# Performance work log

Measured on AMD Instinct MI355X. Metric: run time of the kernel, lower is better.

Reference implementation:

```python
import jax, jax.numpy as jnp
import numpy as np

B, N_IN, D_IN = 64, 2304, 8
J, L = 32, 16  # num_capsules, capsule_dim
ROUTING_ITERS = 3
EPS = 1e-7


def setup_inputs() -> dict:
    key = jax.random.key(0)
    k1, k2 = jax.random.split(key)
    x = jax.random.normal(k1, (B, N_IN, D_IN), dtype=jnp.float32)
    W = jax.random.normal(k2, (N_IN, J, D_IN, L), dtype=jnp.float32) * 0.05
    return {"x": x, "W": W}


def squash(s):
    # s: [B, J, L]
    sq_norm = jnp.sum(jnp.square(s), axis=-1, keepdims=True)
    scale = sq_norm / (1.0 + sq_norm) / jnp.sqrt(sq_norm + EPS)
    return scale * s


def reference(x, W):
    # Faithful to the source: einsum 'bni,njkl->bnjl' sums i and k independently.
    predictions = jnp.einsum('bni,njkl->bnjl', x, W)  # [B, N, J, L]
    b = jnp.zeros((x.shape[0], N_IN, J), dtype=predictions.dtype)
    v = None
    for i in range(ROUTING_ITERS):
        c = jax.nn.softmax(b, axis=2)                       # [B, N, J]
        s = jnp.sum(predictions * c[..., None], axis=1)     # [B, J, L]
        v = squash(s)                                       # [B, J, L]
        if i < ROUTING_ITERS - 1:
            agreement = jnp.einsum('bnjl,bjl->bnj', predictions, v)
            b = b + agreement
    return v
```

## Files before the change

kernel.cpp:

```cpp
#include <hip/hip_runtime.h>

#define B_   64
#define N_   2304
#define J_   32
#define L_   16
#define EPS_ 1e-7f
#define BG   4
#define NSPL 32
#define NSL  72
#define NGRID (NSPL * (B_ / BG))
#define NTHR 1024
#define NT   9
#define STR  20


__global__ __launch_bounds__(256) void prep_kernel(const float* __restrict__ x,
                                                   const float* __restrict__ W,
                                                   float* __restrict__ Ws,
                                                   float* __restrict__ xs_g) {
    const int o = blockIdx.x * 256 + threadIdx.x;
    const int NW4 = N_ * J_ * L_ / 4;
    if (o < NW4) {
        const int n = o >> 7, r = o & 127;
        const float4* base = (const float4*)W + (size_t)n * 1024 + (r >> 2) * 32 + (r & 3);
        float4 s = make_float4(0.f, 0.f, 0.f, 0.f);
#pragma unroll
        for (int k = 0; k < 8; ++k) {
            float4 t = base[k * 4];
            s.x += t.x; s.y += t.y; s.z += t.z; s.w += t.w;
        }
        ((float4*)Ws)[o] = s;
    } else {
        const int q = o - NW4;
        if (q < B_ * N_) {
            const float4* p4 = (const float4*)(x + (size_t)q * 8);
            float4 a = p4[0], c = p4[1];
            xs_g[q] = a.x + a.y + a.z + a.w + c.x + c.y + c.z + c.w;
        }
    }
}

template<int T>
__global__ __launch_bounds__(NTHR) void iter_kernel(const float* __restrict__ Ws,
                                                    const float* __restrict__ xs_g,
                                                    const float* __restrict__ pA,
                                                    float* __restrict__ s0g,
                                                    float* __restrict__ pout) {
    __shared__ float xs_lds[BG * NSL];
    __shared__ float u_lds[BG * 544];
    __shared__ float sred[512 * STR];

    const int tid = threadIdx.x;
    const int sp  = blockIdx.x & (NSPL - 1);
    const int bg  = blockIdx.x >> 5;
    const int bb  = bg * BG;
    const int nb  = sp * NSL;

    if (tid < BG * NSL) {
        const int b4f = tid / NSL, nlf = tid - b4f * NSL;
        xs_lds[tid] = xs_g[(size_t)(bb + b4f) * N_ + nb + nlf];
    }

    if constexpr (T == 1) {
        for (int q = tid; q < BG * 512; q += NTHR) {
            const int ob = q >> 9, jl = q & 511;
            const float* pp = pA + ((size_t)(bb + ob) * NSPL) * 512 + jl;
            float s = 0.f;
#pragma unroll
            for (int s2i = 0; s2i < NSPL; ++s2i) s += pp[s2i * 512];
            if (sp == 0) s0g[(bb + ob) * 512 + jl] = s;
            float sq = s * s;
#pragma unroll
            for (int off = 1; off <= 8; off <<= 1) sq += __shfl_xor(sq, off);
            u_lds[ob * 544 + (jl >> 4) * 17 + (jl & 15)] =
                s * (sq / (1.f + sq) / sqrtf(sq + EPS_));
        }
    } else if constexpr (T == 2) {
        for (int q = tid; q < BG * 512; q += NTHR) {
            const int ob = q >> 9, jl = q & 511;
            float s = s0g[(bb + ob) * 512 + jl];
            float sq = s * s;
#pragma unroll
            for (int off = 1; off <= 8; off <<= 1) sq += __shfl_xor(sq, off);
            float u = s * (sq / (1.f + sq) / sqrtf(sq + EPS_));
            const float* pp = pA + ((size_t)(bb + ob) * NSPL) * 512 + jl;
            float s1 = 0.f;
#pragma unroll
            for (int s2i = 0; s2i < NSPL; ++s2i) s1 += pp[s2i * 512];
            float sq1 = s1 * s1;
#pragma unroll
            for (int off = 1; off <= 8; off <<= 1) sq1 += __shfl_xor(sq1, off);
            u += s1 * (sq1 / (1.f + sq1) / sqrtf(sq1 + EPS_));
            u_lds[ob * 544 + (jl >> 4) * 17 + (jl & 15)] = u;
        }
    }
    __syncthreads();

    const int nl8 = tid >> 7;
    const int b4  = (tid >> 5) & 3;
    const int j   = tid & 31;

    float u4[16];
    if constexpr (T > 0) {
#pragma unroll
        for (int l = 0; l < 16; ++l) u4[l] = u_lds[b4 * 544 + j * 17 + l];
    }

    float acc[16];
#pragma unroll
    for (int l = 0; l < 16; ++l) acc[l] = 0.f;

    const float* wbase = Ws + (size_t)nb * 512 + j * 16;
    const float* xbase = xs_lds + b4 * NSL;

    for (int tile = 0; tile < NT; ++tile) {
        const int nl = tile * 8 + nl8;
        const float4* wr = (const float4*)(wbase + (size_t)nl * 512);
        float4 w0 = wr[0], w1 = wr[1], w2 = wr[2], w3 = wr[3];
        const float xsv = xbase[nl];
        float wgt;
        if constexpr (T == 0) {
            wgt = xsv * (1.f / 32.f);
        } else {
            float lg = w0.x*u4[0]  + w0.y*u4[1]  + w0.z*u4[2]  + w0.w*u4[3]
                     + w1.x*u4[4]  + w1.y*u4[5]  + w1.z*u4[6]  + w1.w*u4[7]
                     + w2.x*u4[8]  + w2.y*u4[9]  + w2.z*u4[10] + w2.w*u4[11]
                     + w3.x*u4[12] + w3.y*u4[13] + w3.z*u4[14] + w3.w*u4[15];
            lg *= xsv;
            float e = __expf(lg);
            float ss = e;
#pragma unroll
            for (int off = 1; off <= 16; off <<= 1) ss += __shfl_xor(ss, off);
            wgt = (e / ss) * xsv;
        }
        acc[0]  += wgt*w0.x; acc[1]  += wgt*w0.y; acc[2]  += wgt*w0.z; acc[3]  += wgt*w0.w;
        acc[4]  += wgt*w1.x; acc[5]  += wgt*w1.y; acc[6]  += wgt*w1.z; acc[7]  += wgt*w1.w;
        acc[8]  += wgt*w2.x; acc[9]  += wgt*w2.y; acc[10] += wgt*w2.z; acc[11] += wgt*w2.w;
        acc[12] += wgt*w3.x; acc[13] += wgt*w3.y; acc[14] += wgt*w3.z; acc[15] += wgt*w3.w;
    }

    if (nl8 >= 4) {
        float* sr = sred + (size_t)(tid - 512) * STR;
        ((float4*)sr)[0] = make_float4(acc[0],  acc[1],  acc[2],  acc[3]);
        ((float4*)sr)[1] = make_float4(acc[4],  acc[5],  acc[6],  acc[7]);
        ((float4*)sr)[2] = make_float4(acc[8],  acc[9],  acc[10], acc[11]);
        ((float4*)sr)[3] = make_float4(acc[12], acc[13], acc[14], acc[15]);
    }
    __syncthreads();
    if (nl8 < 4) {
        float* sr = sred + (size_t)tid * STR;
#pragma unroll
        for (int d = 0; d < 4; ++d) {
            float4 t = ((float4*)sr)[d];
            t.x += acc[d*4+0]; t.y += acc[d*4+1]; t.z += acc[d*4+2]; t.w += acc[d*4+3];
            ((float4*)sr)[d] = t;
        }
    }
    __syncthreads();

    for (int q = tid; q < BG * 512; q += NTHR) {
        const int ob = q >> 9, jl = q & 511;
        const int oj = jl >> 4, ol = jl & 15;
        float s = 0.f;
#pragma unroll
        for (int nl = 0; nl < 4; ++nl)
            s += sred[(size_t)(nl * 128 + ob * 32 + oj) * STR + ol];
        pout[((size_t)(bb + ob) * NSPL + sp) * 512 + jl] = s;
    }
}

__global__ __launch_bounds__(512) void final_kernel(const float* __restrict__ p2,
                                                    float* __restrict__ out) {
    const int g = blockIdx.x * 512 + threadIdx.x;
    const int b = g >> 9, jl = g & 511;
    const float* pp = p2 + ((size_t)b * NSPL) * 512 + jl;
    float s = 0.f;
#pragma unroll
    for (int s2 = 0; s2 < NSPL; ++s2) s += pp[s2 * 512];
    float sq = s * s;
#pragma unroll
    for (int off = 1; off <= 8; off <<= 1) sq += __shfl_xor(sq, off);
    out[g] = s * (sq / (1.f + sq) / sqrtf(sq + EPS_));
}

extern "C" void kernel_launch(void* const* d_in, const int* in_sizes, int n_in,
                              void* d_out, int out_size, void* d_ws, size_t ws_size,
                              hipStream_t stream) {
    const float* x = (const float*)d_in[0];
    const float* W = (const float*)d_in[1];
    float* out = (float*)d_out;

    float* Ws  = (float*)d_ws;
    float* xsg = Ws  + (size_t)N_ * J_ * L_;
    float* p0  = xsg + (size_t)B_ * N_;
    float* p1  = p0  + (size_t)B_ * NSPL * 512;
    float* p2  = p1  + (size_t)B_ * NSPL * 512;
    float* s0  = p2  + (size_t)B_ * NSPL * 512;

    prep_kernel<<<1728, 256, 0, stream>>>(x, W, Ws, xsg);
    iter_kernel<0><<<NGRID, NTHR, 0, stream>>>(Ws, xsg, nullptr, nullptr, p0);
    iter_kernel<1><<<NGRID, NTHR, 0, stream>>>(Ws, xsg, p0, s0, p1);
    iter_kernel<2><<<NGRID, NTHR, 0, stream>>>(Ws, xsg, p1, s0, p2);
    final_kernel<<<64, 512, 0, stream>>>(p2, out);
}
```

Baseline: 91.30 us.

## Halve N-splits, prefetch W rows, fuse final reduction via last-block atomic counter

New measurement: 100.6 us. 1.1x slower.

```diff
diff --git a/kernel.cpp b/kernel.cpp
--- a/kernel.cpp
+++ b/kernel.cpp
@@ -6,19 +6,23 @@
 #define L_   16
 #define EPS_ 1e-7f
 #define BG   4
-#define NSPL 32
-#define NSL  72
-#define NGRID (NSPL * (B_ / BG))
+#define NSPL 16
+#define NSL  144
 #define NTHR 1024
-#define NT   9
+#define NT   18
 #define STR  20
 
 
 __global__ __launch_bounds__(256) void prep_kernel(const float* __restrict__ x,
                                                    const float* __restrict__ W,
                                                    float* __restrict__ Ws,
-                                                   float* __restrict__ xs_g) {
+                                                   float* __restrict__ xs_g,
+                                                   float* __restrict__ p2z,
+                                                   int* __restrict__ ctr) {
     const int o = blockIdx.x * 256 + threadIdx.x;
+    if (o == 0) *ctr = 0;
+    if (o < (B_ * NSPL * 512) / 4)
+        ((float4*)p2z)[o] = make_float4(0.f, 0.f, 0.f, 0.f);
     const int NW4 = N_ * J_ * L_ / 4;
     if (o < NW4) {
         const int n = o >> 7, r = o & 127;
@@ -45,14 +49,18 @@
                                                     const float* __restrict__ xs_g,
                                                     const float* __restrict__ pA,
                                                     float* __restrict__ s0g,
-                                                    float* __restrict__ pout) {
+                                                    float* __restrict__ pout,
+                                                    int* __restrict__ ctr,
+                                                    float* __restrict__ out) {
     __shared__ float xs_lds[BG * NSL];
     __shared__ float u_lds[BG * 544];
     __shared__ float sred[512 * STR];
+    __shared__ int lastflag;
 
     const int tid = threadIdx.x;
-    const int sp  = blockIdx.x & (NSPL - 1);
-    const int bg  = blockIdx.x >> 5;
+    const int blk = blockIdx.x;
+    const int sp  = ((blk & 7) << 1) | ((blk >> 3) & 1);
+    const int bg  = blk >> 4;
     const int bb  = bg * BG;
     const int nb  = sp * NSL;
 
@@ -60,6 +68,14 @@
         const int b4f = tid / NSL, nlf = tid - b4f * NSL;
         xs_lds[tid] = xs_g[(size_t)(bb + b4f) * N_ + nb + nlf];
     }
+
+    const int nl8 = tid >> 7;
+    const int b4  = (tid >> 5) & 3;
+    const int j   = tid & 31;
+    const float* wbase = Ws + (size_t)nb * 512 + j * 16;
+
+    const float4* wr0 = (const float4*)(wbase + (size_t)nl8 * 512);
+    float4 w0 = wr0[0], w1 = wr0[1], w2 = wr0[2], w3 = wr0[3];
 
     if constexpr (T == 1) {
         for (int q = tid; q < BG * 512; q += NTHR) {
@@ -67,7 +83,7 @@
             const float* pp = pA + ((size_t)(bb + ob) * NSPL) * 512 + jl;
             float s = 0.f;
 #pragma unroll
-            for (int s2i = 0; s2i < NSPL; ++s2i) s += pp[s2i * 512];
+            for (int i = 0; i < NSPL; ++i) s += pp[i * 512];
             if (sp == 0) s0g[(bb + ob) * 512 + jl] = s;
             float sq = s * s;
 #pragma unroll
@@ -86,7 +102,7 @@
             const float* pp = pA + ((size_t)(bb + ob) * NSPL) * 512 + jl;
             float s1 = 0.f;
 #pragma unroll
-            for (int s2i = 0; s2i < NSPL; ++s2i) s1 += pp[s2i * 512];
+            for (int i = 0; i < NSPL; ++i) s1 += pp[i * 512];
             float sq1 = s1 * s1;
 #pragma unroll
             for (int off = 1; off <= 8; off <<= 1) sq1 += __shfl_xor(sq1, off);
@@ -96,10 +112,6 @@
     }
     __syncthreads();
 
-    const int nl8 = tid >> 7;
-    const int b4  = (tid >> 5) & 3;
-    const int j   = tid & 31;
-
     float u4[16];
     if constexpr (T > 0) {
 #pragma unroll
@@ -110,14 +122,15 @@
 #pragma unroll
     for (int l = 0; l < 16; ++l) acc[l] = 0.f;
 
-    const float* wbase = Ws + (size_t)nb * 512 + j * 16;
     const float* xbase = xs_lds + b4 * NSL;
 
     for (int tile = 0; tile < NT; ++tile) {
-        const int nl = tile * 8 + nl8;
-        const float4* wr = (const float4*)(wbase + (size_t)nl * 512);
-        float4 w0 = wr[0], w1 = wr[1], w2 = wr[2], w3 = wr[3];
-        const float xsv = xbase[nl];
+        float4 n0, n1, n2, n3;
+        if (tile + 1 < NT) {
+            const float4* nx = (const float4*)(wbase + (size_t)((tile + 1) * 8 + nl8) * 512);
+            n0 = nx[0]; n1 = nx[1]; n2 = nx[2]; n3 = nx[3];
+        }
+        const float xsv = xbase[tile * 8 + nl8];
         float wgt;
         if constexpr (T == 0) {
             wgt = xsv * (1.f / 32.f);
@@ -137,6 +150,7 @@
         acc[4]  += wgt*w1.x; acc[5]  += wgt*w1.y; acc[6]  += wgt*w1.z; acc[7]  += wgt*w1.w;
         acc[8]  += wgt*w2.x; acc[9]  += wgt*w2.y; acc[10] += wgt*w2.z; acc[11] += wgt*w2.w;
         acc[12] += wgt*w3.x; acc[13] += wgt*w3.y; acc[14] += wgt*w3.z; acc[15] += wgt*w3.w;
+        if (tile + 1 < NT) { w0 = n0; w1 = n1; w2 = n2; w3 = n3; }
     }
 
     if (nl8 >= 4) {
@@ -165,22 +179,35 @@
 #pragma unroll
         for (int nl = 0; nl < 4; ++nl)
             s += sred[(size_t)(nl * 128 + ob * 32 + oj) * STR + ol];
-        pout[((size_t)(bb + ob) * NSPL + sp) * 512 + jl] = s;
-    }
-}
-
-__global__ __launch_bounds__(512) void final_kernel(const float* __restrict__ p2,
-                                                    float* __restrict__ out) {
-    const int g = blockIdx.x * 512 + threadIdx.x;
-    const int b = g >> 9, jl = g & 511;
-    const float* pp = p2 + ((size_t)b * NSPL) * 512 + jl;
-    float s = 0.f;
-#pragma unroll
-    for (int s2 = 0; s2 < NSPL; ++s2) s += pp[s2 * 512];
-    float sq = s * s;
-#pragma unroll
-    for (int off = 1; off <= 8; off <<= 1) sq += __shfl_xor(sq, off);
-    out[g] = s * (sq / (1.f + sq) / sqrtf(sq + EPS_));
+        if constexpr (T < 2)
+            pout[((size_t)(bb + ob) * NSPL + sp) * 512 + jl] = s;
+        else
+            unsafeAtomicAdd(&pout[((size_t)(bb + ob) * NSPL + sp) * 512 + jl], s);
+    }
+
+    if constexpr (T == 2) {
+        __syncthreads();
+        if (tid == 0) {
+            int old = __hip_atomic_fetch_add(ctr, 1, __ATOMIC_RELAXED,
+                                             __HIP_MEMORY_SCOPE_AGENT);
+            lastflag = (old == 255) ? 1 : 0;
+        }
+        __syncthreads();
+        if (lastflag) {
+            for (int r = tid; r < B_ * 512; r += NTHR) {
+                const int b = r >> 9, jl = r & 511;
+                float s = 0.f;
+#pragma unroll
+                for (int spp = 0; spp < NSPL; ++spp)
+                    s += __hip_atomic_load(&pout[((size_t)b * NSPL + spp) * 512 + jl],
+                                           __ATOMIC_RELAXED, __HIP_MEMORY_SCOPE_AGENT);
+                float sq = s * s;
+#pragma unroll
+                for (int off = 1; off <= 8; off <<= 1) sq += __shfl_xor(sq, off);
+                out[r] = s * (sq / (1.f + sq) / sqrtf(sq + EPS_));
+            }
+        }
+    }
 }
 
 extern "C" void kernel_launch(void* const* d_in, const int* in_sizes, int n_in,
@@ -196,10 +223,10 @@
     float* p1  = p0  + (size_t)B_ * NSPL * 512;
     float* p2  = p1  + (size_t)B_ * NSPL * 512;
     float* s0  = p2  + (size_t)B_ * NSPL * 512;
-
-    prep_kernel<<<1728, 256, 0, stream>>>(x, W, Ws, xsg);
-    iter_kernel<0><<<NGRID, NTHR, 0, stream>>>(Ws, xsg, nullptr, nullptr, p0);
-    iter_kernel<1><<<NGRID, NTHR, 0, stream>>>(Ws, xsg, p0, s0, p1);
-    iter_kernel<2><<<NGRID, NTHR, 0, stream>>>(Ws, xsg, p1, s0, p2);
-    final_kernel<<<64, 512, 0, stream>>>(p2, out);
+    int*   ctr = (int*)(s0 + (size_t)B_ * 512);
+
+    prep_kernel<<<1728, 256, 0, stream>>>(x, W, Ws, xsg, p2, ctr);
+    iter_kernel<0><<<256, NTHR, 0, stream>>>(Ws, xsg, nullptr, nullptr, p0, nullptr, nullptr);
+    iter_kernel<1><<<256, NTHR, 0, stream>>>(Ws, xsg, p0, s0, p1, nullptr, nullptr);
+    iter_kernel<2><<<256, NTHR, 0, stream>>>(Ws, xsg, p1, s0, p2, ctr, out);
 }
```
